# Performance work log

Hardware: AMD Instinct MI355X
Metric: run time of the kernel (lower is better)

The kernel has to match this reference:

```python
import jax, jax.numpy as jnp
import numpy as np

EPS = 1e-4

@jax.custom_vjp
def bin_active(x):
    # BinActive: sign forward, straight-through (hard-tanh) backward
    return jnp.sign(x)

def _ba_fwd(x):
    return jnp.sign(x), x

def _ba_bwd(x, g):
    return (g * (jnp.abs(x) <= 1.0).astype(g.dtype),)

bin_active.defvjp(_ba_fwd, _ba_bwd)

def norm_bin(x):
    # per-node mean/std (torch .std is unbiased, ddof=1) then binarize
    x = x - jnp.mean(x, axis=1, keepdims=True)
    x = x / (jnp.std(x, axis=1, ddof=1, keepdims=True) + EPS)
    return bin_active(x)

def bin_weight(W):
    # XNOR-style weight binarization: per-output-row scale * sign(W)
    alpha = jnp.mean(jnp.abs(W), axis=1, keepdims=True)
    return alpha * jnp.sign(W)

def bi_sage_conv(x_src, x_tgt, edge_index, W_l, W_r, b):
    # mean-aggregate source messages onto targets, then two binarized linears
    src, dst = edge_index[0], edge_index[1]
    n_tgt = x_tgt.shape[0]
    msg = x_src[src]                                             # [E, F] gather
    agg = jax.ops.segment_sum(msg, dst, num_segments=n_tgt)       # [n_tgt, F]
    cnt = jax.ops.segment_sum(jnp.ones((src.shape[0],), x_src.dtype), dst,
                              num_segments=n_tgt)
    agg = agg / jnp.maximum(cnt, 1.0)[:, None]
    out = agg @ bin_weight(W_l).T + x_tgt @ bin_weight(W_r).T + b
    return out


def setup_inputs() -> dict:
    key = jax.random.key(0)
    ks = jax.random.split(key, 10)
    N0, N1, B = 292864, 11264, 1024
    F_IN, F_HID, F_OUT = 602, 256, 41
    E1, E2 = 281600, 10240
    x = jax.random.normal(ks[0], (N0, F_IN), dtype=jnp.float32)
    # bipartite edges: row0 = source idx in [0, n_src), row1 = target idx in [0, n_tgt)
    ei1 = jnp.stack([jax.random.randint(ks[1], (E1,), 0, N0),
                     jax.random.randint(ks[2], (E1,), 0, N1)]).astype(jnp.int64)
    ei2 = jnp.stack([jax.random.randint(ks[3], (E2,), 0, N1),
                     jax.random.randint(ks[4], (E2,), 0, B)]).astype(jnp.int64)
    s1 = 0.1
    return {
        "x": x,
        "edge_index1": ei1,
        "edge_index2": ei2,
        "n1": N1,
        "n_batch": B,
        "W1_l": s1 * jax.random.normal(ks[5], (F_HID, F_IN), dtype=jnp.float32),
        "W1_r": s1 * jax.random.normal(ks[6], (F_HID, F_IN), dtype=jnp.float32),
        "b1": jnp.zeros((F_HID,), jnp.float32),
        "W2_l": s1 * jax.random.normal(ks[7], (F_OUT, F_HID), dtype=jnp.float32),
        "W2_r": s1 * jax.random.normal(ks[8], (F_OUT, F_HID), dtype=jnp.float32),
        "b2": jnp.zeros((F_OUT,), jnp.float32),
    }


def reference(x, edge_index1, edge_index2, n1, n_batch,
              W1_l, W1_r, b1, W2_l, W2_r, b2):
    # layer 1
    x_t = x[:n1]
    h = bi_sage_conv(norm_bin(x), norm_bin(x_t), edge_index1, W1_l, W1_r, b1)
    h = jax.nn.relu(h)  # dropout p=0.0 -> identity
    # layer 2
    h_t = h[:n_batch]
    out = bi_sage_conv(norm_bin(h), norm_bin(h_t), edge_index2, W2_l, W2_r, b2)
    return jax.nn.log_softmax(out, axis=-1)
```

## Files before the change

### kernel.cpp

```cpp
#include <hip/hip_runtime.h>
#include <hip/hip_bf16.h>
#include <cstdint>
#include <cstddef>

#define CDIV(a,b) (((a)+(b)-1)/(b))

using bf16x8 = __attribute__((ext_vector_type(8))) short;
using f32x4  = __attribute__((ext_vector_type(4))) float;

struct __align__(8) F4 { float x, y, z, w; };
struct __align__(8) F2 { float x, y; };

__device__ __forceinline__ unsigned short sgn_bf16(float s){
  return (s > 0.f) ? 0x3F80u : ((s < 0.f) ? 0xBF80u : 0u);
}

__device__ __forceinline__ int colX(int k){
  int w = k >> 5, b = k & 31;
  if (w < 16){
    int g = w >> 3, wr = w & 7;
    int j = wr >> 1, half = wr & 1;
    return 256*g + 4*(32*half + b) + j;
  }
  int j = w - 16;
  int c = 512 + 4*b + j;
  return (c < 602) ? c : -1;
}
__device__ __forceinline__ int colH(int k){
  int w = k >> 5, b = k & 31;
  int j = w >> 1, half = w & 1;
  return 4*(32*half + b) + j;
}

__global__ void prep_all(const float* __restrict__ W1l, const float* __restrict__ W1r,
                         const float* __restrict__ W2l, const float* __restrict__ W2r,
                         float* __restrict__ aL, float* __restrict__ aR,
                         float* __restrict__ a2L, float* __restrict__ a2R,
                         int* __restrict__ degB, int ndeg,
                         unsigned short* __restrict__ bsgn,
                         unsigned char* __restrict__ mask, int n0, int n1){
  int r = blockIdx.x;
  if (r < 594){
    const float* wr; float* dst; int K;
    if (r < 256){ wr = W1l + (size_t)r*602; dst = aL + r; K = 602; }
    else if (r < 512){ int q = r-256; wr = W1r + (size_t)q*602; dst = aR + q; K = 602; }
    else if (r < 553){ int q = r-512; wr = W2l + (size_t)q*256; dst = a2L + q; K = 256; }
    else { int q = r-553; wr = W2r + (size_t)q*256; dst = a2R + q; K = 256; }
    float s = 0.f;
    for (int k = threadIdx.x; k < K; k += blockDim.x) s += fabsf(wr[k]);
    #pragma unroll
    for (int off = 32; off; off >>= 1) s += __shfl_xor(s, off);
    __shared__ float red[4];
    int wid = threadIdx.x >> 6, lane = threadIdx.x & 63;
    if (lane == 0) red[wid] = s;
    __syncthreads();
    if (threadIdx.x == 0) *dst = (red[0]+red[1]+red[2]+red[3]) / (float)K;
  } else if (r < 642){
    int i = (r - 594)*256 + threadIdx.x;
    if (i < ndeg) degB[i] = 0;
  } else if (r < 1922){
    int idx = (r - 642)*256 + threadIdx.x;
    if (idx < 256*1280){
      int o = idx / 1280, k = idx - o*1280;
      float v = 0.f;
      if (k < 640){ int c = colX(k);       if (c >= 0) v = W1l[(size_t)o*602 + c]; }
      else        { int c = colX(k - 640); if (c >= 0) v = W1r[(size_t)o*602 + c]; }
      bsgn[idx] = sgn_bf16(v);
    }
  } else {
    int i = (r - 1922)*256 + threadIdx.x;
    if (i < n0) mask[i] = (i < n1) ? 1 : 0;
  }
}

__global__ void mark_count(const int* __restrict__ s1, const int* __restrict__ d1, int E1,
                           unsigned char* __restrict__ mask, int* __restrict__ deg1,
                           const int* __restrict__ d2, int E2, int* __restrict__ deg2){
  int e = blockIdx.x*blockDim.x + threadIdx.x;
  if (e < E1){
    mask[s1[e]] = 1;
    atomicAdd(&deg1[d1[e]], 1);
  } else if (e < E1 + E2){
    atomicAdd(&deg2[d2[e - E1]], 1);
  }
}

__global__ void pack_masked(const float* __restrict__ X, uint32_t* __restrict__ P, int nrows,
                            const unsigned char* __restrict__ mask){
  const int row = blockIdx.x*4 + (threadIdx.x >> 6);
  const int lane = threadIdx.x & 63;
  if (row >= nrows) return;
  if (!mask[row]) return;
  const float* xr = X + (size_t)row * 602;
  F4 v0 = *(const F4*)&xr[4*lane];
  F4 v1 = *(const F4*)&xr[256 + 4*lane];
  F4 v2 = {0.f,0.f,0.f,0.f};
  if (lane < 22) v2 = *(const F4*)&xr[512 + 4*lane];
  else if (lane == 22){ F2 t = *(const F2*)&xr[600]; v2.x = t.x; v2.y = t.y; }
  float s = v0.x+v0.y+v0.z+v0.w + v1.x+v1.y+v1.z+v1.w + v2.x+v2.y+v2.z+v2.w;
  #pragma unroll
  for (int off = 32; off; off >>= 1) s += __shfl_xor(s, off);
  const float mean = s / 602.f;
  uint32_t wpos[20], wneg[20];
  {
    float d0 = v0.x - mean, d1v = v0.y - mean, d2v = v0.z - mean, d3 = v0.w - mean;
    unsigned long long b0 = __ballot(d0 > 0.f), b1 = __ballot(d1v > 0.f),
                       b2 = __ballot(d2v > 0.f), b3 = __ballot(d3 > 0.f);
    wpos[0]=(uint32_t)b0; wpos[1]=(uint32_t)(b0>>32); wpos[2]=(uint32_t)b1; wpos[3]=(uint32_t)(b1>>32);
    wpos[4]=(uint32_t)b2; wpos[5]=(uint32_t)(b2>>32); wpos[6]=(uint32_t)b3; wpos[7]=(uint32_t)(b3>>32);
    b0 = __ballot(d0 < 0.f); b1 = __ballot(d1v < 0.f); b2 = __ballot(d2v < 0.f); b3 = __ballot(d3 < 0.f);
    wneg[0]=(uint32_t)b0; wneg[1]=(uint32_t)(b0>>32); wneg[2]=(uint32_t)b1; wneg[3]=(uint32_t)(b1>>32);
    wneg[4]=(uint32_t)b2; wneg[5]=(uint32_t)(b2>>32); wneg[6]=(uint32_t)b3; wneg[7]=(uint32_t)(b3>>32);
  }
  {
    float d0 = v1.x - mean, d1v = v1.y - mean, d2v = v1.z - mean, d3 = v1.w - mean;
    unsigned long long b0 = __ballot(d0 > 0.f), b1 = __ballot(d1v > 0.f),
                       b2 = __ballot(d2v > 0.f), b3 = __ballot(d3 > 0.f);
    wpos[8]=(uint32_t)b0; wpos[9]=(uint32_t)(b0>>32); wpos[10]=(uint32_t)b1; wpos[11]=(uint32_t)(b1>>32);
    wpos[12]=(uint32_t)b2; wpos[13]=(uint32_t)(b2>>32); wpos[14]=(uint32_t)b3; wpos[15]=(uint32_t)(b3>>32);
    b0 = __ballot(d0 < 0.f); b1 = __ballot(d1v < 0.f); b2 = __ballot(d2v < 0.f); b3 = __ballot(d3 < 0.f);
    wneg[8]=(uint32_t)b0; wneg[9]=(uint32_t)(b0>>32); wneg[10]=(uint32_t)b1; wneg[11]=(uint32_t)(b1>>32);
    wneg[12]=(uint32_t)b2; wneg[13]=(uint32_t)(b2>>32); wneg[14]=(uint32_t)b3; wneg[15]=(uint32_t)(b3>>32);
  }
  {
    int base = 4*lane;
    float d0 = v2.x - mean, d1v = v2.y - mean, d2v = v2.z - mean, d3 = v2.w - mean;
    wpos[16] = (uint32_t)__ballot((base+0 < 90) && (d0 > 0.f));
    wpos[17] = (uint32_t)__ballot((base+1 < 90) && (d1v > 0.f));
    wpos[18] = (uint32_t)__ballot((base+2 < 90) && (d2v > 0.f));
    wpos[19] = (uint32_t)__ballot((base+3 < 90) && (d3 > 0.f));
    wneg[16] = (uint32_t)__ballot((base+0 < 90) && (d0 < 0.f));
    wneg[17] = (uint32_t)__ballot((base+1 < 90) && (d1v < 0.f));
    wneg[18] = (uint32_t)__ballot((base+2 < 90) && (d2v < 0.f));
    wneg[19] = (uint32_t)__ballot((base+3 < 90) && (d3 < 0.f));
  }
  if (lane == 0){
    uint32_t* pr = P + (size_t)row * 40;
    #pragma unroll
    for (int q = 0; q < 5; ++q){
      uint4 a; a.x = wpos[4*q]; a.y = wpos[4*q+1]; a.z = wpos[4*q+2]; a.w = wpos[4*q+3];
      *(uint4*)&pr[4*q] = a;
      uint4 b; b.x = wneg[4*q]; b.y = wneg[4*q+1]; b.z = wneg[4*q+2]; b.w = wneg[4*q+3];
      *(uint4*)&pr[20 + 4*q] = b;
    }
  }
}

__global__ void scan_bcat(const int* __restrict__ deg1, int* __restrict__ rs1, int* __restrict__ cur1, int n1,
                          const int* __restrict__ deg2, int* __restrict__ rs2, int* __restrict__ cur2, int n2,
                          const float* __restrict__ W2l, const float* __restrict__ W2r,
                          const float* __restrict__ a2L, const float* __restrict__ a2R,
                          float* __restrict__ Bcat2){
  if (blockIdx.x < 2){
    const int* deg = blockIdx.x ? deg2 : deg1;
    int* rs  = blockIdx.x ? rs2  : rs1;
    int* cur = blockIdx.x ? cur2 : cur1;
    int n    = blockIdx.x ? n2   : n1;
    __shared__ int partial[1024];
    int tid = threadIdx.x;
    int per = CDIV(n, 1024);
    int begin = tid*per; if (begin > n) begin = n;
    int end = begin + per; if (end > n) end = n;
    int s = 0;
    for (int i = begin; i < end; ++i) s += deg[i];
    partial[tid] = s;
    __syncthreads();
    for (int off = 1; off < 1024; off <<= 1){
      int add = (tid >= off) ? partial[tid-off] : 0;
      __syncthreads();
      partial[tid] += add;
      __syncthreads();
    }
    int prefix = (tid == 0) ? 0 : partial[tid-1];
    for (int i = begin; i < end; ++i){ rs[i] = prefix; cur[i] = prefix; prefix += deg[i]; }
    if (tid == 1023) rs[n] = prefix;
  } else {
    int idx = (blockIdx.x - 2)*1024 + threadIdx.x;
    if (idx < 512*41){
      int o = idx % 41, k = idx / 41;
      int c = (k < 256) ? colH(k) : colH(k - 256);
      float w = (k < 256) ? W2l[(size_t)o*256 + c] : W2r[(size_t)o*256 + c];
      float a = (k < 256) ? a2L[o] : a2R[o];
      float sg = (w > 0.f) ? 1.f : ((w < 0.f) ? -1.f : 0.f);
      Bcat2[idx] = a * sg;
    }
  }
}

__global__ void fill_both(const int* __restrict__ s1, const int* __restrict__ d1, int E1,
                          int* __restrict__ cur1, int* __restrict__ esrc1,
                          const int* __restrict__ s2, const int* __restrict__ d2, int E2,
                          int* __restrict__ cur2, int* __restrict__ esrc2){
  int e = blockIdx.x*blockDim.x + threadIdx.x;
  if (e < E1){
    int p = atomicAdd(&cur1[d1[e]], 1);
    esrc1[p] = s1[e];
  } else if (e < E1 + E2){
    int q = e - E1;
    int p = atomicAdd(&cur2[d2[q]], 1);
    esrc2[p] = s2[q];
  }
}

template<int WUSED, int HALF, int STRIDE, int KPAD>
__global__ void aggregate_bf16(const uint32_t* __restrict__ packed,
                               const int* __restrict__ rs, const int* __restrict__ esrc,
                               unsigned short* __restrict__ S, float* __restrict__ invdeg){
  const int t = blockIdx.x;
  const int lane = threadIdx.x;
  const int s0 = rs[t], s1 = rs[t+1];
  uint32_t p[8] = {0,0,0,0,0,0,0,0};
  uint32_t n[8] = {0,0,0,0,0,0,0,0};
  if (lane < WUSED){
    for (int e = s0; e < s1; ++e){
      const uint32_t* pr = packed + (size_t)esrc[e] * STRIDE;
      uint32_t wp = pr[lane];
      uint32_t wn = pr[HALF + lane];
      #pragma unroll
      for (int b = 0; b < 8; ++b){
        p[b] += (wp >> b) & 0x01010101u;
        n[b] += (wn >> b) & 0x01010101u;
      }
    }
  }
  if (lane == 0){
    int deg = s1 - s0;
    invdeg[t] = 1.f / (float)(deg > 0 ? deg : 1);
  }
  if (lane < WUSED){
    unsigned short* sr = S + (size_t)t * KPAD;
    #pragma unroll
    for (int b = 0; b < 8; ++b){
      #pragma unroll
      for (int k = 0; k < 4; ++k){
        int col = 32*lane + b + 8*k;
        int cnt = (int)((p[b] >> (8*k)) & 0xFF) - (int)((n[b] >> (8*k)) & 0xFF);
        float f = (float)cnt;
        sr[col] = (unsigned short)(__float_as_uint(f) >> 16);
      }
    }
  }
}

__global__ __launch_bounds__(256) void gemm1_fused(
    const unsigned short* __restrict__ Sx, const uint32_t* __restrict__ packedX,
    const unsigned short* __restrict__ bsgn, const float* __restrict__ invdeg,
    const float* __restrict__ aL, const float* __restrict__ aR,
    const float* __restrict__ bias, uint32_t* __restrict__ packedH){
  __shared__ __align__(16) char smem[33792];
  unsigned short (*As)[40] = (unsigned short (*)[40])smem;
  unsigned short (*Bs)[40] = (unsigned short (*)[40])(smem + 32*40*2);
  float (*Hs)[264] = (float (*)[264])smem;

  const int tid = threadIdx.x;
  const int lane = tid & 63, wid = tid >> 6;
  const int m0 = blockIdx.x * 32;
  const int frow = lane & 15, fk = (lane >> 4) * 8;
  const int sRow = tid >> 3, sK = (tid & 7) * 4;

  f32x4 acc1[2][4], acc2[2][4];
  #pragma unroll
  for (int i = 0; i < 2; ++i)
    #pragma unroll
    for (int j = 0; j < 4; ++j){ f32x4 z = {0.f,0.f,0.f,0.f}; acc1[i][j] = z; acc2[i][j] = z; }

  const unsigned short* SxRow = Sx + (size_t)(m0 + sRow) * 640;
  const uint32_t* pxRow = packedX + (size_t)(m0 + sRow) * 40;
  const unsigned short* bsgnCol = bsgn + (size_t)tid * 1280;

  for (int kc = 0; kc < 640; kc += 32){
    *(uint2*)&As[sRow][sK] = *(const uint2*)&SxRow[kc + sK];
    *(bf16x8*)&Bs[tid][0]  = *(const bf16x8*)&bsgnCol[kc];
    *(bf16x8*)&Bs[tid][8]  = *(const bf16x8*)&bsgnCol[kc + 8];
    *(bf16x8*)&Bs[tid][16] = *(const bf16x8*)&bsgnCol[kc + 16];
    *(bf16x8*)&Bs[tid][24] = *(const bf16x8*)&bsgnCol[kc + 24];
    __syncthreads();
    bf16x8 a0 = *(bf16x8*)&As[frow][fk];
    bf16x8 a1 = *(bf16x8*)&As[16 + frow][fk];
    #pragma unroll
    for (int nf = 0; nf < 4; ++nf){
      bf16x8 b = *(bf16x8*)&Bs[wid*64 + nf*16 + frow][fk];
      acc1[0][nf] = __builtin_amdgcn_mfma_f32_16x16x32_bf16(a0, b, acc1[0][nf], 0, 0, 0);
      acc1[1][nf] = __builtin_amdgcn_mfma_f32_16x16x32_bf16(a1, b, acc1[1][nf], 0, 0, 0);
    }
    __syncthreads();
  }
  for (int kc = 0; kc < 640; kc += 32){
    int w = kc >> 5;
    {
      uint32_t wp = pxRow[w];
      uint32_t wq = pxRow[20 + w];
      union { unsigned short u[4]; uint2 v; } tmp;
      #pragma unroll
      for (int j = 0; j < 4; ++j){
        int b_ = sK + j;
        tmp.u[j] = ((wp >> b_) & 1) ? 0x3F80u : (((wq >> b_) & 1) ? 0xBF80u : 0u);
      }
      *(uint2*)&As[sRow][sK] = tmp.v;
    }
    *(bf16x8*)&Bs[tid][0]  = *(const bf16x8*)&bsgnCol[640 + kc];
    *(bf16x8*)&Bs[tid][8]  = *(const bf16x8*)&bsgnCol[640 + kc + 8];
    *(bf16x8*)&Bs[tid][16] = *(const bf16x8*)&bsgnCol[640 + kc + 16];
    *(bf16x8*)&Bs[tid][24] = *(const bf16x8*)&bsgnCol[640 + kc + 24];
    __syncthreads();
    bf16x8 a0 = *(bf16x8*)&As[frow][fk];
    bf16x8 a1 = *(bf16x8*)&As[16 + frow][fk];
    #pragma unroll
    for (int nf = 0; nf < 4; ++nf){
      bf16x8 b = *(bf16x8*)&Bs[wid*64 + nf*16 + frow][fk];
      acc2[0][nf] = __builtin_amdgcn_mfma_f32_16x16x32_bf16(a0, b, acc2[0][nf], 0, 0, 0);
      acc2[1][nf] = __builtin_amdgcn_mfma_f32_16x16x32_bf16(a1, b, acc2[1][nf], 0, 0, 0);
    }
    __syncthreads();
  }

  #pragma unroll
  for (int nf = 0; nf < 4; ++nf){
    int gc = wid*64 + nf*16 + frow;
    float al = aL[gc], ar = aR[gc], bb = bias[gc];
    #pragma unroll
    for (int mf = 0; mf < 2; ++mf){
      #pragma unroll
      for (int reg = 0; reg < 4; ++reg){
        int lr = mf*16 + (lane >> 4)*4 + reg;
        float v = invdeg[m0 + lr]*al*acc1[mf][nf][reg] + ar*acc2[mf][nf][reg] + bb;
        Hs[lr][gc] = fmaxf(v, 0.f);
      }
    }
  }
  __syncthreads();

  for (int r = 0; r < 8; ++r){
    int row = wid*8 + r;
    float4 v = *(const float4*)&Hs[row][4*lane];
    float s = v.x + v.y + v.z + v.w;
    #pragma unroll
    for (int off = 32; off; off >>= 1) s += __shfl_xor(s, off);
    float mean = s * (1.f/256.f);
    float d0 = v.x - mean, d1v = v.y - mean, d2v = v.z - mean, d3 = v.w - mean;
    unsigned long long b0 = __ballot(d0 > 0.f), b1 = __ballot(d1v > 0.f),
                       b2 = __ballot(d2v > 0.f), b3 = __ballot(d3 > 0.f);
    uint32_t wpos[8], wneg[8];
    wpos[0]=(uint32_t)b0; wpos[1]=(uint32_t)(b0>>32); wpos[2]=(uint32_t)b1; wpos[3]=(uint32_t)(b1>>32);
    wpos[4]=(uint32_t)b2; wpos[5]=(uint32_t)(b2>>32); wpos[6]=(uint32_t)b3; wpos[7]=(uint32_t)(b3>>32);
    b0 = __ballot(d0 < 0.f); b1 = __ballot(d1v < 0.f); b2 = __ballot(d2v < 0.f); b3 = __ballot(d3 < 0.f);
    wneg[0]=(uint32_t)b0; wneg[1]=(uint32_t)(b0>>32); wneg[2]=(uint32_t)b1; wneg[3]=(uint32_t)(b1>>32);
    wneg[4]=(uint32_t)b2; wneg[5]=(uint32_t)(b2>>32); wneg[6]=(uint32_t)b3; wneg[7]=(uint32_t)(b3>>32);
    if (lane == 0){
      uint32_t* pr = packedH + (size_t)(m0 + row) * 16;
      *(uint4*)&pr[0]  = make_uint4(wpos[0], wpos[1], wpos[2], wpos[3]);
      *(uint4*)&pr[4]  = make_uint4(wpos[4], wpos[5], wpos[6], wpos[7]);
      *(uint4*)&pr[8]  = make_uint4(wneg[0], wneg[1], wneg[2], wneg[3]);
      *(uint4*)&pr[12] = make_uint4(wneg[4], wneg[5], wneg[6], wneg[7]);
    }
  }
}

__global__ void agg_gemm2(const uint32_t* __restrict__ packedH,
                          const int* __restrict__ rs, const int* __restrict__ esrc,
                          const float* __restrict__ Bcat2, const float* __restrict__ bias,
                          float* __restrict__ out){
  const int t = blockIdx.x;
  const int lane = threadIdx.x;
  __shared__ float av[512];
  const int s0 = rs[t], s1 = rs[t+1];
  uint32_t p[8] = {0,0,0,0,0,0,0,0};
  uint32_t n[8] = {0,0,0,0,0,0,0,0};
  if (lane < 8){
    for (int e = s0; e < s1; ++e){
      const uint32_t* pr = packedH + (size_t)esrc[e] * 16;
      uint32_t wp = pr[lane];
      uint32_t wn = pr[8 + lane];
      #pragma unroll
      for (int b = 0; b < 8; ++b){
        p[b] += (wp >> b) & 0x01010101u;
        n[b] += (wn >> b) & 0x01010101u;
      }
    }
    int deg = s1 - s0;
    float inv = 1.f / (float)(deg > 0 ? deg : 1);
    #pragma unroll
    for (int b = 0; b < 8; ++b){
      #pragma unroll
      for (int k = 0; k < 4; ++k){
        int col = 32*lane + b + 8*k;
        int cnt = (int)((p[b] >> (8*k)) & 0xFF) - (int)((n[b] >> (8*k)) & 0xFF);
        av[col] = (float)cnt * inv;
      }
    }
  }
  const uint32_t* pr = packedH + (size_t)t * 16;
  for (int k = lane; k < 256; k += 64){
    int w = k >> 5, b = k & 31;
    av[256 + k] = (float)((pr[w] >> b) & 1) - (float)((pr[8 + w] >> b) & 1);
  }
  __syncthreads();
  bool active = lane < 41;
  float acc = active ? bias[lane] : 0.f;
  for (int k = 0; k < 512; ++k){
    float bw = active ? Bcat2[k*41 + lane] : 0.f;
    acc += av[k] * bw;
  }
  float v = active ? acc : -INFINITY;
  float m = v;
  #pragma unroll
  for (int off = 32; off; off >>= 1) m = fmaxf(m, __shfl_xor(m, off));
  float e = active ? expf(v - m) : 0.f;
  float ssum = e;
  #pragma unroll
  for (int off = 32; off; off >>= 1) ssum += __shfl_xor(ssum, off);
  if (active) out[(size_t)t*41 + lane] = v - m - logf(ssum);
}

extern "C" void kernel_launch(void* const* d_in, const int* in_sizes, int n_in,
                              void* d_out, int out_size, void* d_ws, size_t ws_size,
                              hipStream_t stream){
  (void)n_in; (void)out_size; (void)ws_size;
  const float* x   = (const float*)d_in[0];
  const int*   ei1 = (const int*)d_in[1];
  const int*   ei2 = (const int*)d_in[2];
  const float* W1l = (const float*)d_in[5];
  const float* W1r = (const float*)d_in[6];
  const float* b1  = (const float*)d_in[7];
  const float* W2l = (const float*)d_in[8];
  const float* W2r = (const float*)d_in[9];
  const float* b2  = (const float*)d_in[10];
  float* out = (float*)d_out;

  const int FIN = 602, N1 = 11264, NB = 1024;
  const int N0 = in_sizes[0] / FIN;
  const int E1 = in_sizes[1] / 2;
  const int E2 = in_sizes[2] / 2;

  char* wsb = (char*)d_ws;
  size_t off = 0;
  auto carve = [&](size_t bytes)->void*{
    void* p = wsb + off;
    off = (off + bytes + 255) & ~(size_t)255;
    return p;
  };
  uint32_t* packedX = (uint32_t*)carve((size_t)N0*40*4);
  uint32_t* packedH = (uint32_t*)carve((size_t)N1*16*4);
  unsigned short* Sx = (unsigned short*)carve((size_t)N1*640*2);
  float* invdeg1 = (float*)carve((size_t)N1*4);
  unsigned short* bsgn = (unsigned short*)carve((size_t)256*1280*2);
  float* Bcat2 = (float*)carve((size_t)512*41*4);
  float* aL  = (float*)carve(256*4);
  float* aR  = (float*)carve(256*4);
  float* a2L = (float*)carve(64*4);
  float* a2R = (float*)carve(64*4);
  unsigned char* mask = (unsigned char*)carve((size_t)N0);
  int* degB  = (int*)carve((size_t)(N1+NB)*4);
  int* deg1  = degB;
  int* deg2  = degB + N1;
  int* rs1   = (int*)carve((size_t)(N1+1)*4);
  int* cur1  = (int*)carve((size_t)N1*4);
  int* esrc1 = (int*)carve((size_t)E1*4);
  int* rs2   = (int*)carve((size_t)(NB+1)*4);
  int* cur2  = (int*)carve((size_t)NB*4);
  int* esrc2 = (int*)carve((size_t)E2*4);

  const int maskBlocks = CDIV(N0, 256);
  const int cntBlocks  = CDIV(E1 + E2, 256);

  prep_all<<<1922 + maskBlocks, 256, 0, stream>>>(
      W1l, W1r, W2l, W2r, aL, aR, a2L, a2R, degB, N1 + NB, bsgn, mask, N0, N1);
  mark_count<<<cntBlocks, 256, 0, stream>>>(ei1, ei1 + E1, E1, mask, deg1,
                                            ei2 + E2, E2, deg2);
  pack_masked<<<CDIV(N0, 4), 256, 0, stream>>>(x, packedX, N0, mask);
  scan_bcat<<<2 + CDIV(512*41, 1024), 1024, 0, stream>>>(
      deg1, rs1, cur1, N1, deg2, rs2, cur2, NB, W2l, W2r, a2L, a2R, Bcat2);
  fill_both<<<cntBlocks, 256, 0, stream>>>(ei1, ei1 + E1, E1, cur1, esrc1,
                                           ei2, ei2 + E2, E2, cur2, esrc2);
  aggregate_bf16<20,20,40,640><<<N1, 64, 0, stream>>>(packedX, rs1, esrc1, Sx, invdeg1);
  gemm1_fused<<<N1/32, 256, 0, stream>>>(Sx, packedX, bsgn, invdeg1, aL, aR, b1, packedH);
  agg_gemm2<<<NB, 64, 0, stream>>>(packedH, rs2, esrc2, Bcat2, b2, out);
}
```

Measured before the change: 282.0 us.

## Parallelize edge loops across wave lanes and fuse scan/bcat into pack kernel

Result: no change. 277.3 us (-1.7%).

```diff
diff --git a/kernel.cpp b/kernel.cpp
--- a/kernel.cpp
+++ b/kernel.cpp
@@ -85,9 +85,53 @@
   }
 }
 
-__global__ void pack_masked(const float* __restrict__ X, uint32_t* __restrict__ P, int nrows,
-                            const unsigned char* __restrict__ mask){
-  const int row = blockIdx.x*4 + (threadIdx.x >> 6);
+__global__ void pack_scan_bcat(const float* __restrict__ X, uint32_t* __restrict__ P, int nrows,
+                               const unsigned char* __restrict__ mask, int packBlocks,
+                               const int* __restrict__ deg1, int* __restrict__ rs1, int* __restrict__ cur1, int n1c,
+                               const int* __restrict__ deg2, int* __restrict__ rs2, int* __restrict__ cur2, int n2c,
+                               const float* __restrict__ W2l, const float* __restrict__ W2r,
+                               const float* __restrict__ a2L, const float* __restrict__ a2R,
+                               float* __restrict__ Bcat2){
+  __shared__ int partial[256];
+  const int bid = blockIdx.x;
+  if (bid >= packBlocks){
+    int role = bid - packBlocks;
+    if (role < 2){
+      const int* deg = role ? deg2 : deg1;
+      int* rs  = role ? rs2  : rs1;
+      int* cur = role ? cur2 : cur1;
+      int n    = role ? n2c  : n1c;
+      int tid = threadIdx.x;
+      int per = CDIV(n, 256);
+      int begin = tid*per; if (begin > n) begin = n;
+      int end = begin + per; if (end > n) end = n;
+      int s = 0;
+      for (int i = begin; i < end; ++i) s += deg[i];
+      partial[tid] = s;
+      __syncthreads();
+      for (int off = 1; off < 256; off <<= 1){
+        int add = (tid >= off) ? partial[tid-off] : 0;
+        __syncthreads();
+        partial[tid] += add;
+        __syncthreads();
+      }
+      int prefix = (tid == 0) ? 0 : partial[tid-1];
+      for (int i = begin; i < end; ++i){ rs[i] = prefix; cur[i] = prefix; prefix += deg[i]; }
+      if (tid == 255) rs[n] = prefix;
+    } else {
+      int idx = (role - 2)*256 + threadIdx.x;
+      if (idx < 512*41){
+        int o = idx % 41, k = idx / 41;
+        int c = (k < 256) ? colH(k) : colH(k - 256);
+        float w = (k < 256) ? W2l[(size_t)o*256 + c] : W2r[(size_t)o*256 + c];
+        float a = (k < 256) ? a2L[o] : a2R[o];
+        float sg = (w > 0.f) ? 1.f : ((w < 0.f) ? -1.f : 0.f);
+        Bcat2[idx] = a * sg;
+      }
+    }
+    return;
+  }
+  const int row = bid*4 + (threadIdx.x >> 6);
   const int lane = threadIdx.x & 63;
   if (row >= nrows) return;
   if (!mask[row]) return;
@@ -146,47 +190,6 @@
   }
 }
 
-__global__ void scan_bcat(const int* __restrict__ deg1, int* __restrict__ rs1, int* __restrict__ cur1, int n1,
-                          const int* __restrict__ deg2, int* __restrict__ rs2, int* __restrict__ cur2, int n2,
-                          const float* __restrict__ W2l, const float* __restrict__ W2r,
-                          const float* __restrict__ a2L, const float* __restrict__ a2R,
-                          float* __restrict__ Bcat2){
-  if (blockIdx.x < 2){
-    const int* deg = blockIdx.x ? deg2 : deg1;
-    int* rs  = blockIdx.x ? rs2  : rs1;
-    int* cur = blockIdx.x ? cur2 : cur1;
-    int n    = blockIdx.x ? n2   : n1;
-    __shared__ int partial[1024];
-    int tid = threadIdx.x;
-    int per = CDIV(n, 1024);
-    int begin = tid*per; if (begin > n) begin = n;
-    int end = begin + per; if (end > n) end = n;
-    int s = 0;
-    for (int i = begin; i < end; ++i) s += deg[i];
-    partial[tid] = s;
-    __syncthreads();
-    for (int off = 1; off < 1024; off <<= 1){
-      int add = (tid >= off) ? partial[tid-off] : 0;
-      __syncthreads();
-      partial[tid] += add;
-      __syncthreads();
-    }
-    int prefix = (tid == 0) ? 0 : partial[tid-1];
-    for (int i = begin; i < end; ++i){ rs[i] = prefix; cur[i] = prefix; prefix += deg[i]; }
-    if (tid == 1023) rs[n] = prefix;
-  } else {
-    int idx = (blockIdx.x - 2)*1024 + threadIdx.x;
-    if (idx < 512*41){
-      int o = idx % 41, k = idx / 41;
-      int c = (k < 256) ? colH(k) : colH(k - 256);
-      float w = (k < 256) ? W2l[(size_t)o*256 + c] : W2r[(size_t)o*256 + c];
-      float a = (k < 256) ? a2L[o] : a2R[o];
-      float sg = (w > 0.f) ? 1.f : ((w < 0.f) ? -1.f : 0.f);
-      Bcat2[idx] = a * sg;
-    }
-  }
-}
-
 __global__ void fill_both(const int* __restrict__ s1, const int* __restrict__ d1, int E1,
                           int* __restrict__ cur1, int* __restrict__ esrc1,
                           const int* __restrict__ s2, const int* __restrict__ d2, int E2,
@@ -202,33 +205,42 @@
   }
 }
 
-template<int WUSED, int HALF, int STRIDE, int KPAD>
-__global__ void aggregate_bf16(const uint32_t* __restrict__ packed,
-                               const int* __restrict__ rs, const int* __restrict__ esrc,
-                               unsigned short* __restrict__ S, float* __restrict__ invdeg){
+__global__ void aggregate_v3(const uint32_t* __restrict__ packed,
+                             const int* __restrict__ rs, const int* __restrict__ esrc,
+                             unsigned short* __restrict__ S, float* __restrict__ invdeg){
   const int t = blockIdx.x;
   const int lane = threadIdx.x;
+  const int slot = lane / 20;
+  const int w = lane - slot*20;
   const int s0 = rs[t], s1 = rs[t+1];
+  const bool active = slot < 3;
   uint32_t p[8] = {0,0,0,0,0,0,0,0};
   uint32_t n[8] = {0,0,0,0,0,0,0,0};
-  if (lane < WUSED){
-    for (int e = s0; e < s1; ++e){
-      const uint32_t* pr = packed + (size_t)esrc[e] * STRIDE;
-      uint32_t wp = pr[lane];
-      uint32_t wn = pr[HALF + lane];
-      #pragma unroll
-      for (int b = 0; b < 8; ++b){
-        p[b] += (wp >> b) & 0x01010101u;
-        n[b] += (wn >> b) & 0x01010101u;
-      }
-    }
+  for (int base = s0; base < s1; base += 3){
+    int e = base + slot;
+    uint32_t wp = 0, wn = 0;
+    if (active && e < s1){
+      const uint32_t* pr = packed + (size_t)esrc[e] * 40;
+      wp = pr[w];
+      wn = pr[20 + w];
+    }
+    #pragma unroll
+    for (int b = 0; b < 8; ++b){
+      p[b] += (wp >> b) & 0x01010101u;
+      n[b] += (wn >> b) & 0x01010101u;
+    }
+  }
+  #pragma unroll
+  for (int b = 0; b < 8; ++b){
+    p[b] += __shfl(p[b], lane + 20) + __shfl(p[b], lane + 40);
+    n[b] += __shfl(n[b], lane + 20) + __shfl(n[b], lane + 40);
   }
   if (lane == 0){
     int deg = s1 - s0;
     invdeg[t] = 1.f / (float)(deg > 0 ? deg : 1);
   }
-  if (lane < WUSED){
-    unsigned short* sr = S + (size_t)t * KPAD;
+  if (lane < 20){
+    unsigned short* sr = S + (size_t)t * 640;
     #pragma unroll
     for (int b = 0; b < 8; ++b){
       #pragma unroll
@@ -362,23 +374,33 @@
                           float* __restrict__ out){
   const int t = blockIdx.x;
   const int lane = threadIdx.x;
+  const int slot = lane >> 3, w = lane & 7;
   __shared__ float av[512];
   const int s0 = rs[t], s1 = rs[t+1];
   uint32_t p[8] = {0,0,0,0,0,0,0,0};
   uint32_t n[8] = {0,0,0,0,0,0,0,0};
+  for (int base = s0; base < s1; base += 8){
+    int e = base + slot;
+    uint32_t wp = 0, wn = 0;
+    if (e < s1){
+      const uint32_t* pr = packedH + (size_t)esrc[e] * 16;
+      wp = pr[w];
+      wn = pr[8 + w];
+    }
+    #pragma unroll
+    for (int b = 0; b < 8; ++b){
+      p[b] += (wp >> b) & 0x01010101u;
+      n[b] += (wn >> b) & 0x01010101u;
+    }
+  }
+  #pragma unroll
+  for (int b = 0; b < 8; ++b){
+    p[b] += __shfl_xor(p[b], 8);  p[b] += __shfl_xor(p[b], 16);  p[b] += __shfl_xor(p[b], 32);
+    n[b] += __shfl_xor(n[b], 8);  n[b] += __shfl_xor(n[b], 16);  n[b] += __shfl_xor(n[b], 32);
+  }
+  int deg = s1 - s0;
+  float inv = 1.f / (float)(deg > 0 ? deg : 1);
   if (lane < 8){
-    for (int e = s0; e < s1; ++e){
-      const uint32_t* pr = packedH + (size_t)esrc[e] * 16;
-      uint32_t wp = pr[lane];
-      uint32_t wn = pr[8 + lane];
-      #pragma unroll
-      for (int b = 0; b < 8; ++b){
-        p[b] += (wp >> b) & 0x01010101u;
-        n[b] += (wn >> b) & 0x01010101u;
-      }
-    }
-    int deg = s1 - s0;
-    float inv = 1.f / (float)(deg > 0 ? deg : 1);
     #pragma unroll
     for (int b = 0; b < 8; ++b){
       #pragma unroll
@@ -391,25 +413,25 @@
   }
   const uint32_t* pr = packedH + (size_t)t * 16;
   for (int k = lane; k < 256; k += 64){
-    int w = k >> 5, b = k & 31;
-    av[256 + k] = (float)((pr[w] >> b) & 1) - (float)((pr[8 + w] >> b) & 1);
+    int wq = k >> 5, b = k & 31;
+    av[256 + k] = (float)((pr[wq] >> b) & 1) - (float)((pr[8 + wq] >> b) & 1);
   }
   __syncthreads();
-  bool active = lane < 41;
-  float acc = active ? bias[lane] : 0.f;
+  bool activeO = lane < 41;
+  float acc = activeO ? bias[lane] : 0.f;
   for (int k = 0; k < 512; ++k){
-    float bw = active ? Bcat2[k*41 + lane] : 0.f;
+    float bw = activeO ? Bcat2[k*41 + lane] : 0.f;
     acc += av[k] * bw;
   }
-  float v = active ? acc : -INFINITY;
+  float v = activeO ? acc : -INFINITY;
   float m = v;
   #pragma unroll
   for (int off = 32; off; off >>= 1) m = fmaxf(m, __shfl_xor(m, off));
-  float e = active ? expf(v - m) : 0.f;
+  float e = activeO ? expf(v - m) : 0.f;
   float ssum = e;
   #pragma unroll
   for (int off = 32; off; off >>= 1) ssum += __shfl_xor(ssum, off);
-  if (active) out[(size_t)t*41 + lane] = v - m - logf(ssum);
+  if (activeO) out[(size_t)t*41 + lane] = v - m - logf(ssum);
 }
 
 extern "C" void kernel_launch(void* const* d_in, const int* in_sizes, int n_in,
@@ -462,17 +484,20 @@
 
   const int maskBlocks = CDIV(N0, 256);
   const int cntBlocks  = CDIV(E1 + E2, 256);
+  const int packBlocks = CDIV(N0, 4);
+  const int bcatBlocks = CDIV(512*41, 256);
 
   prep_all<<<1922 + maskBlocks, 256, 0, stream>>>(
       W1l, W1r, W2l, W2r, aL, aR, a2L, a2R, degB, N1 + NB, bsgn, mask, N0, N1);
   mark_count<<<cntBlocks, 256, 0, stream>>>(ei1, ei1 + E1, E1, mask, deg1,
                                             ei2 + E2, E2, deg2);
-  pack_masked<<<CDIV(N0, 4), 256, 0, stream>>>(x, packedX, N0, mask);
-  scan_bcat<<<2 + CDIV(512*41, 1024), 1024, 0, stream>>>(
-      deg1, rs1, cur1, N1, deg2, rs2, cur2, NB, W2l, W2r, a2L, a2R, Bcat2);
+  pack_scan_bcat<<<packBlocks + 2 + bcatBlocks, 256, 0, stream>>>(
+      x, packedX, N0, mask, packBlocks,
+      deg1, rs1, cur1, N1, deg2, rs2, cur2, NB,
+      W2l, W2r, a2L, a2R, Bcat2);
   fill_both<<<cntBlocks, 256, 0, stream>>>(ei1, ei1 + E1, E1, cur1, esrc1,
                                            ei2, ei2 + E2, E2, cur2, esrc2);
-  aggregate_bf16<20,20,40,640><<<N1, 64, 0, stream>>>(packedX, rs1, esrc1, Sx, invdeg1);
+  aggregate_v3<<<N1, 64, 0, stream>>>(packedX, rs1, esrc1, Sx, invdeg1);
   gemm1_fused<<<N1/32, 256, 0, stream>>>(Sx, packedX, bsgn, invdeg1, aL, aR, b1, packedH);
   agg_gemm2<<<NB, 64, 0, stream>>>(packedH, rs2, esrc2, Bcat2, b2, out);
 }
```
